# Kernel optimization log

Measured on AMD Instinct MI355X. Metric: run time of the kernel, lower is better.

## Reference

```python
import jax, jax.numpy as jnp
import numpy as np

B, S, H = 2, 4096, 2048
NH, NKV, HD = 16, 4, 128          # heads, kv heads, head_dim = H // NH
GS_RATIO = 0.25                    # hardcoded in MyAttention.forward
ROPE_BASE = 10000.0


def rotate_half(x):
    h = x.shape[-1] // 2
    return jnp.concatenate((-x[..., h:], x[..., :h]), axis=-1)


def setup_inputs() -> dict:
    key = jax.random.key(0)
    ks = jax.random.split(key, 5)
    g = int(S * GS_RATIO)
    hidden_states = jax.random.normal(ks[0], (B, S, H), jnp.float32)
    position_ids = jnp.tile(jnp.arange(S, dtype=jnp.int32)[None, :], (B, 1))
    # causal additive mask per group window (0 keep, -1e9 masked)
    i = jnp.arange(g)
    causal = i[None, :] <= i[:, None]
    attention_mask = jnp.broadcast_to(
        jnp.where(causal, 0.0, -1e9).astype(jnp.float32)[None, None], (B, 1, g, g)
    )
    sc = 0.02
    Wq = (jax.random.normal(ks[1], (H, NH * HD), jnp.float32) * sc)
    Wk = (jax.random.normal(ks[2], (H, NKV * HD), jnp.float32) * sc)
    Wv = (jax.random.normal(ks[3], (H, NKV * HD), jnp.float32) * sc)
    Wo = (jax.random.normal(ks[4], (NH * HD, H), jnp.float32) * sc)
    return {"hidden_states": hidden_states, "attention_mask": attention_mask,
            "position_ids": position_ids, "Wq": Wq, "Wk": Wk, "Wv": Wv, "Wo": Wo}


def reference(hidden_states, attention_mask, position_ids, Wq, Wk, Wv, Wo):
    B_, S_, H_ = hidden_states.shape
    g = int(S_ * GS_RATIO)
    ng = S_ // g
    n_rep = NH // NKV

    # QKV projections -> (B, heads, S, HD)
    q = (hidden_states @ Wq).reshape(B_, S_, NH, HD).transpose(0, 2, 1, 3)
    k = (hidden_states @ Wk).reshape(B_, S_, NKV, HD).transpose(0, 2, 1, 3)
    v = (hidden_states @ Wv).reshape(B_, S_, NKV, HD).transpose(0, 2, 1, 3)

    # RoPE
    inv_freq = 1.0 / (ROPE_BASE ** (jnp.arange(0, HD, 2, dtype=jnp.float32) / HD))
    t = jnp.arange(S_, dtype=jnp.float32)
    emb = jnp.concatenate([jnp.outer(t, inv_freq)] * 2, axis=-1)  # (S, HD)
    cos = jnp.cos(emb)[position_ids][:, None]  # (B,1,S,HD)
    sin = jnp.sin(emb)[position_ids][:, None]
    q = q * cos + rotate_half(q) * sin
    k = k * cos + rotate_half(k) * sin

    # GQA repeat_kv
    k = jnp.repeat(k, n_rep, axis=1)
    v = jnp.repeat(v, n_rep, axis=1)

    # S2-Attn shift: roll second half of heads by -g/2 along seq, then group
    def shift(x):
        x = jnp.concatenate([x[:, :NH // 2],
                             jnp.roll(x[:, NH // 2:], -g // 2, axis=2)], axis=1)
        return x.transpose(0, 2, 1, 3).reshape(B_ * ng, g, NH, HD).transpose(0, 2, 1, 3)

    q, k, v = shift(q), shift(k), shift(v)

    attn = jnp.einsum('bhqd,bhkd->bhqk', q, k) / np.float32(np.sqrt(HD))
    mask = jnp.tile(attention_mask, (ng, 1, 1, 1))  # (B*ng,1,g,g)
    attn = attn + mask
    attn = jax.nn.softmax(attn.astype(jnp.float32), axis=-1).astype(q.dtype)

    out = jnp.einsum('bhqk,bhkd->bhqd', attn, v)  # (B*ng, NH, g, HD)
    out = out.transpose(0, 2, 1, 3).reshape(B_, S_, NH, HD)
    # undo shift for second half of heads (+g/2 along seq)
    out = jnp.concatenate([out[:, :, :NH // 2],
                           jnp.roll(out[:, :, NH // 2:], g // 2, axis=1)], axis=2)
    out = out.reshape(B_, S_, NH * HD) @ Wo
    return out
```

## Files before the change

kernel.cpp:

```cpp
#include <hip/hip_runtime.h>
#include <math.h>

typedef unsigned short u16;
typedef short bf16x8 __attribute__((ext_vector_type(8)));
typedef float f32x4 __attribute__((ext_vector_type(4)));


__device__ __forceinline__ u16 f2bf(float x) {
  union { float f; unsigned u; } c; c.f = x;
  unsigned r = (c.u + 0x7FFFu + ((c.u >> 16) & 1u)) >> 16;
  return (u16)r;
}
__device__ __forceinline__ float bf2f(u16 x) {
  union { unsigned u; float f; } c; c.u = ((unsigned)x) << 16;
  return c.f;
}

#define GLD16(gp, lp)                                                   \
  __builtin_amdgcn_global_load_lds(                                     \
      (__attribute__((address_space(1))) void*)(gp),                    \
      (__attribute__((address_space(3))) void*)(lp), 16, 0, 0)

#define WAITVM(n) asm volatile("s_waitcnt vmcnt(" #n ")" ::: "memory")
#define BARF  { __builtin_amdgcn_s_barrier(); asm volatile("" ::: "memory"); }

__global__ __launch_bounds__(256) void cast_bf16_vec(
    const float* __restrict__ X, u16* __restrict__ Y) {
  const size_t i = ((size_t)blockIdx.x * 256 + threadIdx.x) * 4;
  float4 v = *(const float4*)(X + i);
  ushort4 o;
  o.x = f2bf(v.x); o.y = f2bf(v.y); o.z = f2bf(v.z); o.w = f2bf(v.w);
  *(ushort4*)(Y + i) = o;
}

__global__ __launch_bounds__(256) void wt_cast(
    const float* __restrict__ W, u16* __restrict__ Wt, int K, int N) {
  const int bk = blockIdx.y * 64;
  const int bn = blockIdx.x * 64;
  __shared__ float T[64 * 65];
  const int tid = threadIdx.x;
  #pragma unroll
  for (int u = 0; u < 16; ++u) {
    int idx = tid + u * 256;
    int kl = idx >> 6, nl = idx & 63;
    T[kl * 65 + nl] = W[(size_t)(bk + kl) * N + bn + nl];
  }
  __syncthreads();
  #pragma unroll
  for (int u = 0; u < 16; ++u) {
    int idx = tid + u * 256;
    int nl = idx >> 6, kl = idx & 63;
    Wt[(size_t)(bn + nl) * K + bk + kl] = f2bf(T[kl * 65 + nl]);
  }
}

__global__ __launch_bounds__(512) void gemm_flow(
    const u16* __restrict__ A, const u16* __restrict__ Bt,
    float* __restrict__ Cf, u16* __restrict__ Cb, int M, int N, int K) {
  __shared__ u16 As[2][2][8192];
  __shared__ u16 Bs[2][2][8192];

  const int tid = threadIdx.x;

  const int gridN = N >> 8;
  const int nwg = gridDim.x * gridDim.y;
  const int orig = blockIdx.y * gridDim.x + blockIdx.x;
  const int wgid = (orig & 7) * (nwg >> 3) + (orig >> 3);
  const int bm = (wgid / gridN) << 8;
  const int bn = (wgid % gridN) << 8;

  const int w = tid >> 6, lane = tid & 63;
  const int col = lane & 15, quad = lane >> 4;
  const int wm = w >> 2, wn = w & 3;

  const int r0 = tid >> 3;
  const int c0 = tid & 7;
  const int scc8 = ((c0 ^ (r0 & 7)) << 3);
  const u16* aH00 = A  + (size_t)(bm + r0)       * K + scc8;
  const u16* aH01 = A  + (size_t)(bm + 64 + r0)  * K + scc8;
  const u16* aH10 = A  + (size_t)(bm + 128 + r0) * K + scc8;
  const u16* aH11 = A  + (size_t)(bm + 192 + r0) * K + scc8;
  const u16* bH00 = Bt + (size_t)(bn + r0)       * K + scc8;
  const u16* bH01 = Bt + (size_t)(bn + 64 + r0)  * K + scc8;
  const u16* bH10 = Bt + (size_t)(bn + 128 + r0) * K + scc8;
  const u16* bH11 = Bt + (size_t)(bn + 192 + r0) * K + scc8;

#define STG(P0, P1, DST, t_) {                                   \
    GLD16((P0) + (size_t)(t_) * 64, (DST) + tid * 8);            \
    GLD16((P1) + (size_t)(t_) * 64, (DST) + 4096 + tid * 8); }

  const int cx = col & 7;
  const int kc0 = (quad ^ cx) << 3;
  const int kc1 = ((4 + quad) ^ cx) << 3;
  const int arow = (wm * 64 + col) << 6;
  const int brow = (wn * 32 + col) << 6;

#define RDA(DST, qa, CUR) { _Pragma("unroll") for (int i = 0; i < 4; ++i) { \
    DST[i][0] = *(const bf16x8*)&As[CUR][qa][arow + i * 1024 + kc0];        \
    DST[i][1] = *(const bf16x8*)&As[CUR][qa][arow + i * 1024 + kc1]; } }
#define RDB(DST, qb, CUR) { _Pragma("unroll") for (int j = 0; j < 2; ++j) { \
    DST[j][0] = *(const bf16x8*)&Bs[CUR][qb][brow + j * 1024 + kc0];        \
    DST[j][1] = *(const bf16x8*)&Bs[CUR][qb][brow + j * 1024 + kc1]; } }
#define MMA(ACC, AF, BF) { _Pragma("unroll") for (int ks = 0; ks < 2; ++ks) \
    _Pragma("unroll") for (int i = 0; i < 4; ++i)                           \
    _Pragma("unroll") for (int j = 0; j < 2; ++j)                           \
      ACC[i][j] = __builtin_amdgcn_mfma_f32_16x16x32_bf16(                  \
          AF[i][ks], BF[j][ks], ACC[i][j], 0, 0, 0); }

  f32x4 acc00[4][2], acc01[4][2], acc11[4][2], acc10[4][2];
  #pragma unroll
  for (int i = 0; i < 4; ++i)
    #pragma unroll
    for (int j = 0; j < 2; ++j) {
      acc00[i][j] = (f32x4)(0.0f); acc01[i][j] = (f32x4)(0.0f);
      acc11[i][j] = (f32x4)(0.0f); acc10[i][j] = (f32x4)(0.0f);
    }

  const int NT = K >> 6;

  STG(aH00, aH01, &As[0][0][0], 0);
  STG(bH00, bH01, &Bs[0][0][0], 0);
  STG(bH10, bH11, &Bs[0][1][0], 0);
  STG(aH10, aH11, &As[0][1][0], 0);
  WAITVM(0); BARF;

  for (int t = 0; t < NT; ++t) {
    const int cur = t & 1, nxt = cur ^ 1;

    if (t + 1 < NT) {
      STG(aH00, aH01, &As[nxt][0][0], t + 1);
      STG(bH00, bH01, &Bs[nxt][0][0], t + 1);
      STG(bH10, bH11, &Bs[nxt][1][0], t + 1);
      STG(aH10, aH11, &As[nxt][1][0], t + 1);
    }

    {
      bf16x8 af[4][2], b0[2][2], b1[2][2];
      RDA(af, 0, cur); RDB(b0, 0, cur); RDB(b1, 1, cur);
      __builtin_amdgcn_s_setprio(1);
      MMA(acc00, af, b0);
      MMA(acc01, af, b1);
      __builtin_amdgcn_s_setprio(0);
      RDA(af, 1, cur);
      __builtin_amdgcn_s_setprio(1);
      MMA(acc11, af, b1);
      MMA(acc10, af, b0);
      __builtin_amdgcn_s_setprio(0);
    }

    if (t + 1 < NT) WAITVM(0);
    BARF;
  }

#define WR(ACC, qa, qb) { _Pragma("unroll") for (int i = 0; i < 4; ++i)    \
    _Pragma("unroll") for (int j = 0; j < 2; ++j)                          \
    _Pragma("unroll") for (int r = 0; r < 4; ++r) {                        \
      const int rr = bm + (qa) * 128 + wm * 64 + i * 16 + quad * 4 + r;    \
      const int cc = bn + (qb) * 128 + wn * 32 + j * 16 + col;             \
      if (Cb) Cb[(size_t)rr * N + cc] = f2bf(ACC[i][j][r]);                \
      else    Cf[(size_t)rr * N + cc] = ACC[i][j][r]; } }
  WR(acc00, 0, 0); WR(acc01, 0, 1); WR(acc11, 1, 1); WR(acc10, 1, 0);
#undef WR
#undef RDA
#undef RDB
#undef MMA
#undef STG
}

__global__ __launch_bounds__(256) void rope_qkv(
    u16* __restrict__ QKV, const int* __restrict__ pos) {
  const unsigned idx = blockIdx.x * 256 + threadIdx.x;
  const int d = idx & 63;
  const unsigned rest = idx >> 6;
  const int hh = rest % 20;
  const unsigned bs = rest / 20;

  const int colbase = (hh < 16) ? hh * 128 : 2048 + (hh - 16) * 128;
  u16* p = QKV + (size_t)bs * 3072 + colbase + d;
  const float x0 = bf2f(p[0]);
  const float x1 = bf2f(p[64]);
  const float t = (float)pos[bs];
  const float inv_freq = __expf((float)d * -0.14391156509676332f);
  float s, c;
  __sincosf(t * inv_freq, &s, &c);
  const float sc = (hh < 16) ? 0.08838834764831845f : 1.0f;
  p[0]  = f2bf((x0 * c - x1 * s) * sc);
  p[64] = f2bf((x1 * c + x0 * s) * sc);
}

__global__ __launch_bounds__(256) void v_transpose(
    const u16* __restrict__ QKV, u16* __restrict__ Vt) {
  const int bid = blockIdx.x;
  const int st = bid & 63;
  const int kvh = (bid >> 6) & 3;
  const int b = bid >> 8;
  __shared__ u16 T[64 * 136];
  const int tid = threadIdx.x;
  #pragma unroll
  for (int u = 0; u < 4; ++u) {
    int idx = tid + u * 256;
    int sl = idx >> 4, ch = idx & 15;
    *(uint4*)&T[sl * 136 + ch * 8] =
        *(const uint4*)(QKV + ((size_t)(b * 4096 + st * 64 + sl)) * 3072 + 2560 + kvh * 128 + ch * 8);
  }
  __syncthreads();
  #pragma unroll
  for (int u = 0; u < 32; ++u) {
    int idx = tid + u * 256;
    int d = idx >> 6, sl = idx & 63;
    Vt[((size_t)((b * 4 + kvh) * 128 + d)) * 4096 + st * 64 + sl] = T[sl * 136 + d];
  }
}

__global__ __launch_bounds__(256) void attn_mfma(
    const u16* __restrict__ QKV, const u16* __restrict__ Vt,
    u16* __restrict__ Ob) {
  __shared__ u16 Ks[2][64 * 128];
  __shared__ u16 Vs[2][128 * 64];
  __shared__ u16 Ps[4][16 * 72];

  const int bid = blockIdx.x;
  const int qt = 15 - (bid & 15);
  const int h  = (bid >> 4) & 15;
  const int gi = (bid >> 8) & 3;
  const int b  = bid >> 10;

  const int tid = threadIdx.x;
  const int w = tid >> 6, lane = tid & 63;
  const int col = lane & 15, quad = lane >> 4;

  const int shift = (h >= 8) ? 512 : 0;
  const int base_s = gi * 1024;
  const int kvh = h >> 2;

  const int kco8 = ((tid & 15) ^ ((tid >> 4) & 7)) << 3;
  const int vco8 = ((tid & 7) ^ ((tid >> 3) & 7)) << 3;
  const size_t krow = (size_t)(tid >> 4) * 3072 + kco8;
  const size_t vrow = (size_t)(tid >> 3) * 4096 + vco8;
  u16* kdst = &Ks[0][0] + tid * 8;
  u16* vdst = &Vs[0][0] + tid * 8;
  const size_t vbase = (size_t)((b * 4 + kvh) * 128) * 4096;
  const u16* kgb = QKV + (size_t)b * 4096 * 3072 + 2048 + kvh * 128;

#define ASTAGE(kt_, buf_) {                                               \
    const int sk_ = (base_s + (kt_) * 64 + shift) & 4095;                 \
    const u16* ks_ = kgb + (size_t)sk_ * 3072;                            \
    const u16* vs_ = Vt + vbase + sk_;                                    \
    GLD16(ks_ + krow,             kdst + (buf_) * 8192);                  \
    GLD16(ks_ + krow + 16 * 3072, kdst + (buf_) * 8192 + 2048);           \
    GLD16(ks_ + krow + 32 * 3072, kdst + (buf_) * 8192 + 4096);           \
    GLD16(ks_ + krow + 48 * 3072, kdst + (buf_) * 8192 + 6144);           \
    GLD16(vs_ + vrow,             vdst + (buf_) * 8192);                  \
    GLD16(vs_ + vrow + 32 * 4096, vdst + (buf_) * 8192 + 2048);           \
    GLD16(vs_ + vrow + 64 * 4096, vdst + (buf_) * 8192 + 4096);           \
    GLD16(vs_ + vrow + 96 * 4096, vdst + (buf_) * 8192 + 6144);           \
  }

  const int sq0 = (base_s + qt * 64 + shift) & 4095;
  {
    const u16* qsrc = QKV + ((size_t)(b * 4096 + sq0)) * 3072 + h * 128;
    GLD16(qsrc + krow,             kdst);
    GLD16(qsrc + krow + 16 * 3072, kdst + 2048);
    GLD16(qsrc + krow + 32 * 3072, kdst + 4096);
    GLD16(qsrc + krow + 48 * 3072, kdst + 6144);
  }
  asm volatile("s_waitcnt vmcnt(0)" ::: "memory");
  __builtin_amdgcn_s_barrier();
  asm volatile("" ::: "memory");

  const int cxor = col & 7;
  bf16x8 aq[4];
  {
    const int qr = w * 16 + col;
    #pragma unroll
    for (int kk = 0; kk < 4; ++kk)
      aq[kk] = *(const bf16x8*)&Ks[0][qr * 128 + ((((kk << 2) + quad) ^ cxor) << 3)];
  }
  asm volatile("s_waitcnt lgkmcnt(0)" ::: "memory");
  __builtin_amdgcn_s_barrier();
  asm volatile("" ::: "memory");

  ASTAGE(0, 0);

  f32x4 o[8];
  #pragma unroll
  for (int jd = 0; jd < 8; ++jd) o[jd] = (f32x4)(0.0f);
  float lp[4] = {0.0f, 0.0f, 0.0f, 0.0f};

  u16* Pw = &Ps[w][0];
  const int qrow_l = w * 16 + quad * 4;

  for (int kt = 0; kt <= qt; ++kt) {
    const u16* Kc = &Ks[kt & 1][0];
    const u16* Vc = &Vs[kt & 1][0];
    const bool pf = (kt < qt);
    if (pf) ASTAGE(kt + 1, (kt + 1) & 1);
    if (pf) asm volatile("s_waitcnt vmcnt(8)" ::: "memory");
    else    asm volatile("s_waitcnt vmcnt(0)" ::: "memory");
    __builtin_amdgcn_s_barrier();
    asm volatile("" ::: "memory");

    f32x4 scv[4];
    #pragma unroll
    for (int j = 0; j < 4; ++j) scv[j] = (f32x4)(0.0f);
    __builtin_amdgcn_s_setprio(1);
    #pragma unroll
    for (int kk = 0; kk < 4; ++kk) {
      #pragma unroll
      for (int j = 0; j < 4; ++j) {
        bf16x8 bk = *(const bf16x8*)&Kc[(16 * j + col) * 128 + ((((kk << 2) + quad) ^ cxor) << 3)];
        scv[j] = __builtin_amdgcn_mfma_f32_16x16x32_bf16(aq[kk], bk, scv[j], 0, 0, 0);
      }
    }
    __builtin_amdgcn_s_setprio(0);

    const bool last = (kt == qt);
    #pragma unroll
    for (int j = 0; j < 4; ++j) {
      #pragma unroll
      for (int r = 0; r < 4; ++r) {
        float p = __expf(scv[j][r]);
        if (last && (16 * j + col) > (qrow_l + r)) p = 0.0f;
        lp[r] += p;
        Pw[(quad * 4 + r) * 72 + 16 * j + col] = f2bf(p);
      }
    }

    __builtin_amdgcn_s_setprio(1);
    #pragma unroll
    for (int ks = 0; ks < 2; ++ks) {
      bf16x8 ap = *(const bf16x8*)&Pw[col * 72 + ks * 32 + quad * 8];
      #pragma unroll
      for (int jd = 0; jd < 8; ++jd) {
        bf16x8 bv = *(const bf16x8*)&Vc[(16 * jd + col) * 64 + ((((ks << 2) + quad) ^ cxor) << 3)];
        o[jd] = __builtin_amdgcn_mfma_f32_16x16x32_bf16(ap, bv, o[jd], 0, 0, 0);
      }
    }
    __builtin_amdgcn_s_setprio(0);

    asm volatile("" ::: "memory");
    __builtin_amdgcn_s_barrier();
  }
#undef ASTAGE

  #pragma unroll
  for (int r = 0; r < 4; ++r) {
    lp[r] += __shfl_xor(lp[r], 1, 64);
    lp[r] += __shfl_xor(lp[r], 2, 64);
    lp[r] += __shfl_xor(lp[r], 4, 64);
    lp[r] += __shfl_xor(lp[r], 8, 64);
  }

  #pragma unroll
  for (int r = 0; r < 4; ++r) {
    const int qg = qt * 64 + w * 16 + quad * 4 + r;
    const int sq = (base_s + qg + shift) & 4095;
    u16* dst = Ob + ((size_t)(b * 4096 + sq)) * 2048 + h * 128;
    const float inv = 1.0f / lp[r];
    #pragma unroll
    for (int jd = 0; jd < 8; ++jd)
      dst[16 * jd + col] = f2bf(o[jd][r] * inv);
  }
}

extern "C" void kernel_launch(void* const* d_in, const int* in_sizes, int n_in,
                              void* d_out, int out_size, void* d_ws, size_t ws_size,
                              hipStream_t stream) {
  const float* hs = (const float*)d_in[0];
  const int*   pos = (const int*)d_in[2];
  const float* Wq = (const float*)d_in[3];
  const float* Wk = (const float*)d_in[4];
  const float* Wv = (const float*)d_in[5];
  const float* Wo = (const float*)d_in[6];

  char* ws = (char*)d_ws;
  u16* hsb   = (u16*)ws; ws += (size_t)8192 * 2048 * 2;
  u16* Wqkvt = (u16*)ws; ws += (size_t)3072 * 2048 * 2;
  u16* Wot   = (u16*)ws; ws += (size_t)2048 * 2048 * 2;
  u16* QKVb  = (u16*)ws; ws += (size_t)8192 * 3072 * 2;
  u16* Vtt   = (u16*)ws; ws += (size_t)2 * 4 * 128 * 4096 * 2;
  u16* Obh   = (u16*)ws; ws += (size_t)8192 * 2048 * 2;

  dim3 blk(256);

  cast_bf16_vec<<<16384, blk, 0, stream>>>(hs, hsb);
  wt_cast<<<dim3(32, 32), blk, 0, stream>>>(Wq, Wqkvt, 2048, 2048);
  wt_cast<<<dim3(8, 32),  blk, 0, stream>>>(Wk, Wqkvt + (size_t)2048 * 2048, 2048, 512);
  wt_cast<<<dim3(8, 32),  blk, 0, stream>>>(Wv, Wqkvt + (size_t)2560 * 2048, 2048, 512);
  wt_cast<<<dim3(32, 32), blk, 0, stream>>>(Wo, Wot, 2048, 2048);

  gemm_flow<<<dim3(12, 32), dim3(512), 0, stream>>>(hsb, Wqkvt, nullptr, QKVb, 8192, 3072, 2048);

  rope_qkv<<<40960, blk, 0, stream>>>(QKVb, pos);

  v_transpose<<<512, blk, 0, stream>>>(QKVb, Vtt);

  attn_mfma<<<2048, blk, 0, stream>>>(QKVb, Vtt, Obh);

  gemm_flow<<<dim3(8, 32), dim3(512), 0, stream>>>(Obh, Wot, (float*)d_out, nullptr, 8192, 2048, 2048);
}
```

Baseline: 508.1 us.

## Fuse prep and RoPE/V-transpose launches; add dedicated 128x256 QKV GEMM

Merges the hidden-state cast and the four weight transpose-casts into one prep kernel, and merges RoPE with the V transpose into one kernel, cutting the number of launches. Replaces the generic 256x256-tile GEMM for the QKV projection with a dedicated 128x256-tile kernel that launches 768 workgroups instead of 384, aiming for better wave balance across CUs. The new GEMM uses a simpler double-buffered loop, which may schedule loads and MFMAs less efficiently than the original interleaved pipeline.

```diff
diff --git a/kernel.cpp b/kernel.cpp
--- a/kernel.cpp
+++ b/kernel.cpp
@@ -24,39 +24,146 @@
 #define WAITVM(n) asm volatile("s_waitcnt vmcnt(" #n ")" ::: "memory")
 #define BARF  { __builtin_amdgcn_s_barrier(); asm volatile("" ::: "memory"); }
 
-__global__ __launch_bounds__(256) void cast_bf16_vec(
-    const float* __restrict__ X, u16* __restrict__ Y) {
-  const size_t i = ((size_t)blockIdx.x * 256 + threadIdx.x) * 4;
-  float4 v = *(const float4*)(X + i);
-  ushort4 o;
-  o.x = f2bf(v.x); o.y = f2bf(v.y); o.z = f2bf(v.z); o.w = f2bf(v.w);
-  *(ushort4*)(Y + i) = o;
-}
-
-__global__ __launch_bounds__(256) void wt_cast(
-    const float* __restrict__ W, u16* __restrict__ Wt, int K, int N) {
-  const int bk = blockIdx.y * 64;
-  const int bn = blockIdx.x * 64;
+__global__ __launch_bounds__(256) void prep(
+    const float* __restrict__ hs, u16* __restrict__ hsb,
+    const float* __restrict__ Wq, const float* __restrict__ Wk,
+    const float* __restrict__ Wv, const float* __restrict__ Wo,
+    u16* __restrict__ Wqkvt, u16* __restrict__ Wot) {
+  const int b = blockIdx.x;
+  const int tid = threadIdx.x;
+
+  if (b < 16384) {
+    const size_t i = ((size_t)b * 256 + tid) * 4;
+    float4 v = *(const float4*)(hs + i);
+    ushort4 o;
+    o.x = f2bf(v.x); o.y = f2bf(v.y); o.z = f2bf(v.z); o.w = f2bf(v.w);
+    *(ushort4*)(hsb + i) = o;
+    return;
+  }
+
   __shared__ float T[64 * 65];
+  const float* W; u16* Wt; int N, bx, by;
+  int idx = b - 16384;
+  if (idx < 1024)      {              W = Wq; Wt = Wqkvt;                        N = 2048; bx = idx & 31; by = idx >> 5; }
+  else if (idx < 1280) { idx -= 1024; W = Wk; Wt = Wqkvt + (size_t)2048 * 2048;  N = 512;  bx = idx & 7;  by = idx >> 3; }
+  else if (idx < 1536) { idx -= 1280; W = Wv; Wt = Wqkvt + (size_t)2560 * 2048;  N = 512;  bx = idx & 7;  by = idx >> 3; }
+  else                 { idx -= 1536; W = Wo; Wt = Wot;                          N = 2048; bx = idx & 31; by = idx >> 5; }
+  const int K = 2048;
+  const int bk = by * 64, bn = bx * 64;
+  #pragma unroll
+  for (int u = 0; u < 16; ++u) {
+    int id2 = tid + u * 256;
+    int kl = id2 >> 6, nl = id2 & 63;
+    T[kl * 65 + nl] = W[(size_t)(bk + kl) * N + bn + nl];
+  }
+  __syncthreads();
+  #pragma unroll
+  for (int u = 0; u < 16; ++u) {
+    int id2 = tid + u * 256;
+    int nl = id2 >> 6, kl = id2 & 63;
+    Wt[(size_t)(bn + nl) * K + bk + kl] = f2bf(T[kl * 65 + nl]);
+  }
+}
+
+__global__ __launch_bounds__(512) void gemm_qkv(
+    const u16* __restrict__ A, const u16* __restrict__ Bt,
+    u16* __restrict__ Cb) {
+  const int K = 2048, N = 3072, NT = 32;
+  __shared__ u16 As[2][8192];
+  __shared__ u16 Bs[2][16384];
+
   const int tid = threadIdx.x;
-  #pragma unroll
-  for (int u = 0; u < 16; ++u) {
-    int idx = tid + u * 256;
-    int kl = idx >> 6, nl = idx & 63;
-    T[kl * 65 + nl] = W[(size_t)(bk + kl) * N + bn + nl];
-  }
-  __syncthreads();
-  #pragma unroll
-  for (int u = 0; u < 16; ++u) {
-    int idx = tid + u * 256;
-    int nl = idx >> 6, kl = idx & 63;
-    Wt[(size_t)(bn + nl) * K + bk + kl] = f2bf(T[kl * 65 + nl]);
-  }
+
+  const int orig = blockIdx.x;
+  const int wgid = (orig & 7) * 96 + (orig >> 3);
+  const int bm = (wgid / 12) * 128;
+  const int bn = (wgid % 12) * 256;
+
+  const int w = tid >> 6, lane = tid & 63;
+  const int col = lane & 15, quad = lane >> 4;
+  const int wm = w >> 2, wn = w & 3;
+
+  const int r0 = tid >> 3;
+  const int c0 = tid & 7;
+  const int scc8 = ((c0 ^ (r0 & 7)) << 3);
+  const u16* aS0 = A + (size_t)(bm + r0) * K + scc8;
+  const u16* aS1 = A + (size_t)(bm + 64 + r0) * K + scc8;
+  const u16* bS0 = Bt + (size_t)(bn + r0) * K + scc8;
+  const u16* bS1 = Bt + (size_t)(bn + 64 + r0) * K + scc8;
+  const u16* bS2 = Bt + (size_t)(bn + 128 + r0) * K + scc8;
+  const u16* bS3 = Bt + (size_t)(bn + 192 + r0) * K + scc8;
+
+#define STGQ(buf, t_) {                                            \
+    GLD16(aS0 + (size_t)(t_) * 64, &As[buf][0] + tid * 8);         \
+    GLD16(aS1 + (size_t)(t_) * 64, &As[buf][4096] + tid * 8);      \
+    GLD16(bS0 + (size_t)(t_) * 64, &Bs[buf][0] + tid * 8);         \
+    GLD16(bS1 + (size_t)(t_) * 64, &Bs[buf][4096] + tid * 8);      \
+    GLD16(bS2 + (size_t)(t_) * 64, &Bs[buf][8192] + tid * 8);      \
+    GLD16(bS3 + (size_t)(t_) * 64, &Bs[buf][12288] + tid * 8); }
+
+  const int cx = col & 7;
+  const int kc0 = (quad ^ cx) << 3;
+  const int kc1 = ((4 + quad) ^ cx) << 3;
+  const int arow = (wm * 64 + col) << 6;
+  const int brow = (wn * 64 + col) << 6;
+
+  f32x4 acc[4][4];
+  #pragma unroll
+  for (int i = 0; i < 4; ++i)
+    #pragma unroll
+    for (int j = 0; j < 4; ++j) acc[i][j] = (f32x4)(0.0f);
+
+  STGQ(0, 0);
+  WAITVM(0); BARF;
+
+  for (int t = 0; t < NT; ++t) {
+    const int cur = t & 1, nxt = cur ^ 1;
+    if (t + 1 < NT) STGQ(nxt, t + 1);
+
+    {
+      bf16x8 af[4][2], bfv[4][2];
+      #pragma unroll
+      for (int i = 0; i < 4; ++i) {
+        af[i][0] = *(const bf16x8*)&As[cur][arow + i * 1024 + kc0];
+        af[i][1] = *(const bf16x8*)&As[cur][arow + i * 1024 + kc1];
+      }
+      #pragma unroll
+      for (int j = 0; j < 4; ++j) {
+        bfv[j][0] = *(const bf16x8*)&Bs[cur][brow + j * 1024 + kc0];
+        bfv[j][1] = *(const bf16x8*)&Bs[cur][brow + j * 1024 + kc1];
+      }
+      __builtin_amdgcn_s_setprio(1);
+      #pragma unroll
+      for (int ks = 0; ks < 2; ++ks)
+        #pragma unroll
+        for (int i = 0; i < 4; ++i)
+          #pragma unroll
+          for (int j = 0; j < 4; ++j)
+            acc[i][j] = __builtin_amdgcn_mfma_f32_16x16x32_bf16(
+                af[i][ks], bfv[j][ks], acc[i][j], 0, 0, 0);
+      __builtin_amdgcn_s_setprio(0);
+    }
+
+    if (t + 1 < NT) WAITVM(0);
+    BARF;
+  }
+
+  #pragma unroll
+  for (int i = 0; i < 4; ++i)
+    #pragma unroll
+    for (int j = 0; j < 4; ++j)
+      #pragma unroll
+      for (int r = 0; r < 4; ++r) {
+        const int rr = bm + wm * 64 + 16 * i + quad * 4 + r;
+        const int cc = bn + wn * 64 + 16 * j + col;
+        Cb[(size_t)rr * N + cc] = f2bf(acc[i][j][r]);
+      }
+#undef STGQ
 }
 
 __global__ __launch_bounds__(512) void gemm_flow(
     const u16* __restrict__ A, const u16* __restrict__ Bt,
-    float* __restrict__ Cf, u16* __restrict__ Cb, int M, int N, int K) {
+    float* __restrict__ Cf, int M, int N, int K) {
   __shared__ u16 As[2][2][8192];
   __shared__ u16 Bs[2][2][8192];
 
@@ -157,8 +264,7 @@
     _Pragma("unroll") for (int r = 0; r < 4; ++r) {                        \
       const int rr = bm + (qa) * 128 + wm * 64 + i * 16 + quad * 4 + r;    \
       const int cc = bn + (qb) * 128 + wn * 32 + j * 16 + col;             \
-      if (Cb) Cb[(size_t)rr * N + cc] = f2bf(ACC[i][j][r]);                \
-      else    Cf[(size_t)rr * N + cc] = ACC[i][j][r]; } }
+      Cf[(size_t)rr * N + cc] = ACC[i][j][r]; } }
   WR(acc00, 0, 0); WR(acc01, 0, 1); WR(acc11, 1, 1); WR(acc10, 1, 0);
 #undef WR
 #undef RDA
@@ -167,48 +273,51 @@
 #undef STG
 }
 
-__global__ __launch_bounds__(256) void rope_qkv(
-    u16* __restrict__ QKV, const int* __restrict__ pos) {
-  const unsigned idx = blockIdx.x * 256 + threadIdx.x;
-  const int d = idx & 63;
-  const unsigned rest = idx >> 6;
-  const int hh = rest % 20;
-  const unsigned bs = rest / 20;
-
-  const int colbase = (hh < 16) ? hh * 128 : 2048 + (hh - 16) * 128;
-  u16* p = QKV + (size_t)bs * 3072 + colbase + d;
-  const float x0 = bf2f(p[0]);
-  const float x1 = bf2f(p[64]);
-  const float t = (float)pos[bs];
-  const float inv_freq = __expf((float)d * -0.14391156509676332f);
-  float s, c;
-  __sincosf(t * inv_freq, &s, &c);
-  const float sc = (hh < 16) ? 0.08838834764831845f : 1.0f;
-  p[0]  = f2bf((x0 * c - x1 * s) * sc);
-  p[64] = f2bf((x1 * c + x0 * s) * sc);
-}
-
-__global__ __launch_bounds__(256) void v_transpose(
-    const u16* __restrict__ QKV, u16* __restrict__ Vt) {
-  const int bid = blockIdx.x;
+__global__ __launch_bounds__(256) void rope_vt(
+    u16* __restrict__ QKV, const int* __restrict__ pos,
+    u16* __restrict__ Vt) {
+  const int b = blockIdx.x;
+  const int tid = threadIdx.x;
+
+  if (b < 40960) {
+    const unsigned idx = (unsigned)b * 256 + tid;
+    const int d = idx & 63;
+    const unsigned rest = idx >> 6;
+    const int hh = rest % 20;
+    const unsigned bs = rest / 20;
+
+    const int colbase = (hh < 16) ? hh * 128 : 2048 + (hh - 16) * 128;
+    u16* p = QKV + (size_t)bs * 3072 + colbase + d;
+    const float x0 = bf2f(p[0]);
+    const float x1 = bf2f(p[64]);
+    const float t = (float)pos[bs];
+    const float inv_freq = __expf((float)d * -0.14391156509676332f);
+    float s, c;
+    __sincosf(t * inv_freq, &s, &c);
+    const float sc = (hh < 16) ? 0.08838834764831845f : 1.0f;
+    p[0]  = f2bf((x0 * c - x1 * s) * sc);
+    p[64] = f2bf((x1 * c + x0 * s) * sc);
+    return;
+  }
+
+  __shared__ u16 T[64 * 136];
+  const int bid = b - 40960;
   const int st = bid & 63;
   const int kvh = (bid >> 6) & 3;
-  const int b = bid >> 8;
-  __shared__ u16 T[64 * 136];
-  const int tid = threadIdx.x;
+  const int bb = bid >> 8;
   #pragma unroll
   for (int u = 0; u < 4; ++u) {
     int idx = tid + u * 256;
     int sl = idx >> 4, ch = idx & 15;
     *(uint4*)&T[sl * 136 + ch * 8] =
-        *(const uint4*)(QKV + ((size_t)(b * 4096 + st * 64 + sl)) * 3072 + 2560 + kvh * 128 + ch * 8);
+        *(const uint4*)(QKV + ((size_t)(bb * 4096 + st * 64 + sl)) * 3072 + 2560 + kvh * 128 + ch * 8);
   }
   __syncthreads();
   #pragma unroll
   for (int u = 0; u < 32; ++u) {
     int idx = tid + u * 256;
     int d = idx >> 6, sl = idx & 63;
-    Vt[((size_t)((b * 4 + kvh) * 128 + d)) * 4096 + st * 64 + sl] = T[sl * 136 + d];
+    Vt[((size_t)((bb * 4 + kvh) * 128 + d)) * 4096 + st * 64 + sl] = T[sl * 136 + d];
   }
 }
 
@@ -381,21 +490,13 @@
   u16* Vtt   = (u16*)ws; ws += (size_t)2 * 4 * 128 * 4096 * 2;
   u16* Obh   = (u16*)ws; ws += (size_t)8192 * 2048 * 2;
 
-  dim3 blk(256);
-
-  cast_bf16_vec<<<16384, blk, 0, stream>>>(hs, hsb);
-  wt_cast<<<dim3(32, 32), blk, 0, stream>>>(Wq, Wqkvt, 2048, 2048);
-  wt_cast<<<dim3(8, 32),  blk, 0, stream>>>(Wk, Wqkvt + (size_t)2048 * 2048, 2048, 512);
-  wt_cast<<<dim3(8, 32),  blk, 0, stream>>>(Wv, Wqkvt + (size_t)2560 * 2048, 2048, 512);
-  wt_cast<<<dim3(32, 32), blk, 0, stream>>>(Wo, Wot, 2048, 2048);
-
-  gemm_flow<<<dim3(12, 32), dim3(512), 0, stream>>>(hsb, Wqkvt, nullptr, QKVb, 8192, 3072, 2048);
-
-  rope_qkv<<<40960, blk, 0, stream>>>(QKVb, pos);
-
-  v_transpose<<<512, blk, 0, stream>>>(QKVb, Vtt);
-
-  attn_mfma<<<2048, blk, 0, stream>>>(QKVb, Vtt, Obh);
-
-  gemm_flow<<<dim3(8, 32), dim3(512), 0, stream>>>(Obh, Wot, (float*)d_out, nullptr, 8192, 2048, 2048);
-}
+  prep<<<18944, dim3(256), 0, stream>>>(hs, hsb, Wq, Wk, Wv, Wo, Wqkvt, Wot);
+
+  gemm_qkv<<<768, dim3(512), 0, stream>>>(hsb, Wqkvt, QKVb);
+
+  rope_vt<<<41472, dim3(256), 0, stream>>>(QKVb, pos, Vtt);
+
+  attn_mfma<<<2048, dim3(256), 0, stream>>>(QKVb, Vtt, Obh);
+
+  gemm_flow<<<dim3(8, 32), dim3(512), 0, stream>>>(Obh, Wot, (float*)d_out, 8192, 2048, 2048);
+}
```

Measured after the change: 500.4 us. No clear change (-1.5%).
